# Kernel tuning notes

Hardware: AMD Instinct MI355X
Metric: run time of the kernel (lower is better)

Reference implementation:

```python
import jax, jax.numpy as jnp
import numpy as np

STEPS, BATCH = 2048, 512
INPUT_DIM = 16          # climate features after stripping flow channel
STORE_DIM = 8           # number of conceptual stores S
HIDDEN = 128
SLOW = 2                # SLOW_STORE index
RAIN_IDX = 0            # rain column within sliced climate inputs
OUT_DIM = STORE_DIM * (STORE_DIM + 2)   # flow_between_stores=True -> 80
IN_DIM_FLOWNET = INPUT_DIM + STORE_DIM  # 24


def setup_inputs() -> dict:
    key = jax.random.key(0)
    ks = jax.random.split(key, 10)
    hyd_input = jax.random.uniform(ks[0], (STEPS, BATCH, 1 + INPUT_DIM), dtype=jnp.float32)
    s = 0.05
    W0 = jax.random.normal(ks[1], (HIDDEN, IN_DIM_FLOWNET), dtype=jnp.float32) * s
    b0 = jax.random.normal(ks[2], (HIDDEN,), dtype=jnp.float32) * s
    W1 = jax.random.normal(ks[3], (HIDDEN, HIDDEN), dtype=jnp.float32) * s
    b1 = jax.random.normal(ks[4], (HIDDEN,), dtype=jnp.float32) * s
    W_in = jax.random.normal(ks[5], (STORE_DIM + 1, HIDDEN), dtype=jnp.float32) * s
    b_in = jax.random.normal(ks[6], (STORE_DIM + 1,), dtype=jnp.float32) * s
    W_out = jax.random.normal(ks[7], (OUT_DIM, HIDDEN), dtype=jnp.float32) * s
    b_out = jax.random.normal(ks[8], (OUT_DIM,), dtype=jnp.float32) * s - 3.0  # bias.data -= 3
    return {"hyd_input": hyd_input, "W0": W0, "b0": b0, "W1": W1, "b1": b1,
            "W_in": W_in, "b_in": b_in, "W_out": W_out, "b_out": b_out}


def reference(hyd_input, W0, b0, W1, b1, W_in, b_in, W_out, b_out):
    S = STORE_DIM
    flow = hyd_input[:, :, 0]          # [T, B] observed flow
    x = hyd_input[:, :, 1:]            # [T, B, F] climate forcings
    rain = x[:, :, RAIN_IDX]           # [T, B]
    # correct_init_baseflow: 25th percentile of observed flow over time, per batch elem
    baseflow = jnp.percentile(flow, 25.0, axis=0)  # [B]

    B = x.shape[1]
    stores0 = jnp.zeros((B, S), dtype=hyd_input.dtype).at[:, 1].set(1.0)  # init_stores

    def step(stores, inp):
        x_t, rain_t, is_first = inp
        # flownet: (num_layers=2) Linear -> ReLU (dropout is eval-mode identity)
        h = jnp.concatenate([x_t, 0.01 * stores], axis=1)      # [B, F+S]
        h = jax.nn.relu(h @ W0.T + b0)
        h = jax.nn.relu(h @ W1.T + b1)
        # inflow gating (softmax over S+1): distribute rain into stores
        a = jax.nn.softmax(h @ W_in.T + b_in, axis=-1)          # [B, S+1]
        stores = stores + a[:, 1:] * rain_t[:, None]
        # outflow fluxes (sigmoid), S*(S+2) = inter-store | escape | flow
        b = jax.nn.sigmoid(h @ W_out.T + b_out)                 # [B, S*(S+2)]
        # sequential inter-store transfers (order matters; S is small/fixed)
        for d in range(S):
            fb = b[:, d * S:(d + 1) * S] * stores               # [B, S]
            stores = (stores - fb).at[:, d].add(fb.sum(axis=1))
        escape = b[:, -2 * S:-S] * stores
        stores = stores - escape
        b_flow = b[:, -S:]
        flow_distn = b_flow * stores
        stores = stores - flow_distn
        # at i==0: overwrite slow store from baseflow / outflow coeff
        corrected = stores.at[:, SLOW].set(baseflow / jnp.maximum(b_flow[:, SLOW], 1e-5))
        stores = jnp.where(is_first, corrected, stores)
        return stores, flow_distn.sum(axis=1)

    is_first = jnp.arange(x.shape[0]) == 0
    _, flows = jax.lax.scan(step, stores0, (x, rain, is_first))
    return flows  # [T, B]
```

## Files before the change

kernel.cpp:

```cpp
#include <hip/hip_runtime.h>
#include <hip/hip_bf16.h>
#include <math.h>

#define STEPS 2048
#define BATCH 512

typedef __attribute__((ext_vector_type(8))) short short8;
typedef __attribute__((ext_vector_type(4))) short short4v;
typedef __attribute__((ext_vector_type(2))) short short2v;
typedef __attribute__((ext_vector_type(4))) float f32x4;

__device__ __forceinline__ short f2bf(float f) {
    union { float f; unsigned u; } v; v.f = f;
    unsigned u = v.u;
    return (short)((u + 0x7FFFu + ((u >> 16) & 1u)) >> 16);
}
__device__ __forceinline__ short2v pk2(float a, float b) {
    __hip_bfloat162 h = __float22bfloat162_rn(make_float2(a, b));
    union { __hip_bfloat162 h; short2v s; } u; u.h = h; return u.s;
}

__global__ __launch_bounds__(256) void baseflow_kernel(
    const float* __restrict__ hyd, float* __restrict__ bf)
{
    __shared__ float arr[STEPS];
    const int b = blockIdx.x;
    const int tid = threadIdx.x;
    for (int t = tid; t < STEPS; t += 256)
        arr[t] = hyd[(size_t)(t * BATCH + b) * 17];
    __syncthreads();
    for (int k = 2; k <= STEPS; k <<= 1) {
        for (int j = k >> 1; j > 0; j >>= 1) {
            for (int i = tid; i < STEPS; i += 256) {
                int ixj = i ^ j;
                if (ixj > i) {
                    float a = arr[i], c = arr[ixj];
                    bool up = ((i & k) == 0);
                    if (up ? (a > c) : (a < c)) { arr[i] = c; arr[ixj] = a; }
                }
            }
            __syncthreads();
        }
    }
    if (tid == 0) bf[b] = arr[511] + 0.75f * (arr[512] - arr[511]);
}

__global__ __launch_bounds__(256, 1) void hyd_step_kernel(
    const float* __restrict__ hyd,
    const float* __restrict__ W0,  const float* __restrict__ b0,
    const float* __restrict__ W1,  const float* __restrict__ b1,
    const float* __restrict__ Win, const float* __restrict__ bin,
    const float* __restrict__ Wout,const float* __restrict__ bout,
    const float* __restrict__ baseflow,
    float* __restrict__ out)
{
    __shared__ __align__(16) short h1F[256 * 8];
    __shared__ __align__(16) short h2F[256 * 8];
    __shared__ __align__(16) short ringX[16 * 4 * 8];
    __shared__ float ringR[16][2];
    __shared__ __align__(16) float hb[2][96];

    const int tid  = threadIdx.x;
    const int blk  = blockIdx.x;
    const int lane = tid & 63;
    const int wv   = tid >> 6;
    const int cn   = lane & 15;
    const int cg   = lane >> 4;
    const int col  = lane & 1;

    for (int i = tid; i < 256 * 8; i += 256) { h1F[i] = 0; h2F[i] = 0; }

    short8 a0[2]; f32x4 c0[2];
    short8 a1[2][4]; f32x4 c1[2];
    short8 ah[2][4]; f32x4 ch[2];
    #pragma unroll
    for (int i = 0; i < 2; ++i) {
        const int mt = 2 * wv + i;
        const int row = mt * 16 + cn;
        #pragma unroll
        for (int j = 0; j < 8; ++j) {
            int k = cg * 8 + j;
            a0[i][j] = (k < 24) ? f2bf(W0[row * 24 + k]) : (short)0;
        }
        #pragma unroll
        for (int kt = 0; kt < 4; ++kt)
            #pragma unroll
            for (int j = 0; j < 8; ++j)
                a1[i][kt][j] = f2bf(W1[row * 128 + kt * 32 + cg * 8 + j]);
        #pragma unroll
        for (int r = 0; r < 4; ++r) {
            int m = mt * 16 + cg * 4 + r;
            c0[i][r] = b0[m];
            c1[i][r] = b1[m];
        }
    }
    const int nht = (wv < 2) ? 2 : 1;
    int htile[2];
    htile[0] = (wv < 2) ? 2 * wv : 4 + (wv - 2);
    htile[1] = (wv < 2) ? 2 * wv + 1 : htile[0];
    #pragma unroll
    for (int i = 0; i < 2; ++i) {
        const int ht = htile[i];
        const int row = ht * 16 + cn;
        #pragma unroll
        for (int kt = 0; kt < 4; ++kt)
            #pragma unroll
            for (int j = 0; j < 8; ++j) {
                int k = kt * 32 + cg * 8 + j;
                float w = 0.f;
                if (row < 9)       w = Win[row * 128 + k];
                else if (row < 89) w = Wout[(row - 9) * 128 + k];
                ah[i][kt][j] = f2bf(w);
            }
        #pragma unroll
        for (int r = 0; r < 4; ++r) {
            int m = ht * 16 + cg * 4 + r;
            float bb = 0.f;
            if (m < 9)       bb = bin[m];
            else if (m < 89) bb = bout[m - 9];
            ch[i][r] = bb;
        }
    }

    float sreg[8];
    #pragma unroll
    for (int j = 0; j < 8; ++j) sreg[j] = (j == 1) ? 1.f : 0.f;
    const float bfv = baseflow[blk * 2 + col];
    short8 spack;
    #pragma unroll
    for (int jj = 0; jj < 4; ++jj) {
        short2v p = pk2(0.01f * sreg[2 * jj], 0.01f * sreg[2 * jj + 1]);
        spack[2 * jj] = p[0]; spack[2 * jj + 1] = p[1];
    }

    for (int tb = 0; tb < STEPS; tb += 16) {
        if (tid < 64) {
            const int tp = tid >> 2, c = (tid >> 1) & 1, g2 = tid & 1;
            const float* p = hyd + ((size_t)(tb + tp) * BATCH + blk * 2 + c) * 17 + 1 + g2 * 8;
            float v0 = p[0], v1 = p[1], v2 = p[2], v3 = p[3];
            float v4 = p[4], v5 = p[5], v6 = p[6], v7 = p[7];
            short8 w;
            short2v q0 = pk2(v0, v1), q1 = pk2(v2, v3), q2 = pk2(v4, v5), q3 = pk2(v6, v7);
            w[0] = q0[0]; w[1] = q0[1]; w[2] = q1[0]; w[3] = q1[1];
            w[4] = q2[0]; w[5] = q2[1]; w[6] = q3[0]; w[7] = q3[1];
            *(short8*)&ringX[(tp * 4 + g2 * 2 + c) * 8] = w;
        } else if (tid < 96) {
            const int l = tid - 64, tp = l >> 1, c = l & 1;
            ringR[tp][c] = hyd[((size_t)(tb + tp) * BATCH + blk * 2 + c) * 17 + 1];
        }
        __syncthreads();

        for (int tt = 0; tt < 16; ++tt) {
            const int t = tb + tt;

            const float rain = ringR[tt][col];

            short8 bfrag = 0;
            if (cn < 2) {
                if (cg < 2)        bfrag = *(const short8*)&ringX[(tt * 4 + cg * 2 + cn) * 8];
                else if (cg == 2)  bfrag = spack;
            }
            #pragma unroll
            for (int i = 0; i < 2; ++i) {
                f32x4 acc = __builtin_amdgcn_mfma_f32_16x16x32_bf16(a0[i], bfrag, c0[i], 0, 0, 0);
                if (cn < 2) {
                    int m0 = (2 * wv + i) * 16 + cg * 4;
                    short4v p;
                    short2v pa = pk2(fmaxf(acc[0], 0.f), fmaxf(acc[1], 0.f));
                    short2v pb = pk2(fmaxf(acc[2], 0.f), fmaxf(acc[3], 0.f));
                    p[0] = pa[0]; p[1] = pa[1]; p[2] = pb[0]; p[3] = pb[1];
                    *(short4v*)&h1F[((m0 >> 3) * 16 + cn) * 8 + (m0 & 7)] = p;
                }
            }
            __syncthreads();

            short8 bf1[4];
            #pragma unroll
            for (int kt = 0; kt < 4; ++kt)
                bf1[kt] = *(const short8*)&h1F[(kt * 64 + lane) * 8];
            #pragma unroll
            for (int i = 0; i < 2; ++i) {
                f32x4 acc = c1[i];
                #pragma unroll
                for (int kt = 0; kt < 4; ++kt)
                    acc = __builtin_amdgcn_mfma_f32_16x16x32_bf16(a1[i][kt], bf1[kt], acc, 0, 0, 0);
                if (cn < 2) {
                    int m0 = (2 * wv + i) * 16 + cg * 4;
                    short4v p;
                    short2v pa = pk2(fmaxf(acc[0], 0.f), fmaxf(acc[1], 0.f));
                    short2v pb = pk2(fmaxf(acc[2], 0.f), fmaxf(acc[3], 0.f));
                    p[0] = pa[0]; p[1] = pa[1]; p[2] = pb[0]; p[3] = pb[1];
                    *(short4v*)&h2F[((m0 >> 3) * 16 + cn) * 8 + (m0 & 7)] = p;
                }
            }
            __syncthreads();

            short8 bf2[4];
            #pragma unroll
            for (int kt = 0; kt < 4; ++kt)
                bf2[kt] = *(const short8*)&h2F[(kt * 64 + lane) * 8];
            #pragma unroll
            for (int i = 0; i < 2; ++i) {
                if (i < nht) {
                    f32x4 acc = ch[i];
                    #pragma unroll
                    for (int kt = 0; kt < 4; ++kt)
                        acc = __builtin_amdgcn_mfma_f32_16x16x32_bf16(ah[i][kt], bf2[kt], acc, 0, 0, 0);
                    if (cn < 2) {
                        const int ht = htile[i];
                        float4 o;
                        #pragma unroll
                        for (int r = 0; r < 4; ++r) {
                            int m = ht * 16 + cg * 4 + r;
                            float v = acc[r];
                            bool isl = (m < 9);
                            float em = __expf(isl ? v : -v);
                            float res = isl ? em : __builtin_amdgcn_rcpf(1.f + em);
                            ((float*)&o)[r] = res;
                        }
                        *(float4*)&hb[cn][ht * 16 + cg * 4] = o;
                    }
                }
            }
            __syncthreads();

            {
                float gv[92];
                const float4* hp = (const float4*)&hb[col][0];
                #pragma unroll
                for (int c2 = 0; c2 < 23; ++c2)
                    ((float4*)gv)[c2] = hp[c2];

                float den = ((gv[0] + gv[1]) + (gv[2] + gv[3])) +
                            ((gv[4] + gv[5]) + (gv[6] + gv[7])) + gv[8];
                float rr = rain * __builtin_amdgcn_rcpf(den);
                #pragma unroll
                for (int j = 0; j < 8; ++j) sreg[j] += gv[1 + j] * rr;

                #pragma unroll
                for (int d = 0; d < 8; ++d) {
                    float fb[8];
                    #pragma unroll
                    for (int j = 0; j < 8; ++j) fb[j] = gv[9 + d * 8 + j] * sreg[j];
                    float fs = ((fb[0] + fb[1]) + (fb[2] + fb[3])) +
                               ((fb[4] + fb[5]) + (fb[6] + fb[7]));
                    #pragma unroll
                    for (int j = 0; j < 8; ++j) sreg[j] -= fb[j];
                    sreg[d] += fs;
                }
                #pragma unroll
                for (int j = 0; j < 8; ++j) sreg[j] -= gv[73 + j] * sreg[j];
                float fd[8];
                #pragma unroll
                for (int j = 0; j < 8; ++j) fd[j] = gv[81 + j] * sreg[j];
                float fsum = ((fd[0] + fd[1]) + (fd[2] + fd[3])) +
                             ((fd[4] + fd[5]) + (fd[6] + fd[7]));
                #pragma unroll
                for (int j = 0; j < 8; ++j) sreg[j] -= fd[j];
                if (t == 0) sreg[2] = bfv / fmaxf(gv[83], 1e-5f);

                #pragma unroll
                for (int jj = 0; jj < 4; ++jj) {
                    short2v p = pk2(0.01f * sreg[2 * jj], 0.01f * sreg[2 * jj + 1]);
                    spack[2 * jj] = p[0]; spack[2 * jj + 1] = p[1];
                }
                if (tid < 2) out[(size_t)t * BATCH + blk * 2 + tid] = fsum;
            }
        }
    }
}

extern "C" void kernel_launch(void* const* d_in, const int* in_sizes, int n_in,
                              void* d_out, int out_size, void* d_ws, size_t ws_size,
                              hipStream_t stream)
{
    const float* hyd  = (const float*)d_in[0];
    const float* W0   = (const float*)d_in[1];
    const float* b0   = (const float*)d_in[2];
    const float* W1   = (const float*)d_in[3];
    const float* b1   = (const float*)d_in[4];
    const float* Win  = (const float*)d_in[5];
    const float* bin  = (const float*)d_in[6];
    const float* Wout = (const float*)d_in[7];
    const float* bout = (const float*)d_in[8];
    float* out = (float*)d_out;
    float* bf  = (float*)d_ws;

    baseflow_kernel<<<BATCH, 256, 0, stream>>>(hyd, bf);
    hyd_step_kernel<<<BATCH / 2, 256, 0, stream>>>(
        hyd, W0, b0, W1, b1, Win, bin, Wout, bout, bf, out);
}
```

Before: 3.380 ms.

## Process one batch element per block and spread store updates across lanes

Each block now handles a single batch column instead of two, doubling the grid and allowing two blocks per CU. The idea is to overlap the latency-bound recurrent chains of independent blocks on each CU. The sequential inter-store transfer loop moves from one thread doing all eight stores to eight lanes, one store each, with xor-shuffle reductions. The packed bf16 store vector is rebuilt from lane shuffles. The risks are lower MFMA column utilisation, more shuffle latency in the serial per-step path, and register pressure from the two-block launch bound.

Measured after the change: 4.384 ms. 29.7% more time.

```diff
diff --git a/kernel.cpp b/kernel.cpp
--- a/kernel.cpp
+++ b/kernel.cpp
@@ -14,6 +14,9 @@
     union { float f; unsigned u; } v; v.f = f;
     unsigned u = v.u;
     return (short)((u + 0x7FFFu + ((u >> 16) & 1u)) >> 16);
+}
+__device__ __forceinline__ unsigned f2bfu(float f) {
+    return (unsigned)(unsigned short)f2bf(f);
 }
 __device__ __forceinline__ short2v pk2(float a, float b) {
     __hip_bfloat162 h = __float22bfloat162_rn(make_float2(a, b));
@@ -45,7 +48,7 @@
     if (tid == 0) bf[b] = arr[511] + 0.75f * (arr[512] - arr[511]);
 }
 
-__global__ __launch_bounds__(256, 1) void hyd_step_kernel(
+__global__ __launch_bounds__(256, 2) void hyd_step_kernel(
     const float* __restrict__ hyd,
     const float* __restrict__ W0,  const float* __restrict__ b0,
     const float* __restrict__ W1,  const float* __restrict__ b1,
@@ -56,17 +59,17 @@
 {
     __shared__ __align__(16) short h1F[256 * 8];
     __shared__ __align__(16) short h2F[256 * 8];
-    __shared__ __align__(16) short ringX[16 * 4 * 8];
-    __shared__ float ringR[16][2];
-    __shared__ __align__(16) float hb[2][96];
+    __shared__ __align__(16) short ringX[16 * 2 * 8];
+    __shared__ float ringR[16];
+    __shared__ __align__(16) float hb[96];
 
     const int tid  = threadIdx.x;
-    const int blk  = blockIdx.x;
+    const int b    = blockIdx.x;
     const int lane = tid & 63;
     const int wv   = tid >> 6;
     const int cn   = lane & 15;
     const int cg   = lane >> 4;
-    const int col  = lane & 1;
+    const int j8   = lane & 7;
 
     for (int i = tid; i < 256 * 8; i += 256) { h1F[i] = 0; h2F[i] = 0; }
 
@@ -122,54 +125,49 @@
         }
     }
 
-    float sreg[8];
-    #pragma unroll
-    for (int j = 0; j < 8; ++j) sreg[j] = (j == 1) ? 1.f : 0.f;
-    const float bfv = baseflow[blk * 2 + col];
-    short8 spack;
-    #pragma unroll
-    for (int jj = 0; jj < 4; ++jj) {
-        short2v p = pk2(0.01f * sreg[2 * jj], 0.01f * sreg[2 * jj + 1]);
-        spack[2 * jj] = p[0]; spack[2 * jj + 1] = p[1];
-    }
+    float sj = (j8 == 1) ? 1.f : 0.f;
+    const float bfv = baseflow[b];
+    unsigned sp0 = (f2bfu(0.01f) << 16);
+    unsigned sp1 = 0, sp2 = 0, sp3 = 0;
 
     for (int tb = 0; tb < STEPS; tb += 16) {
-        if (tid < 64) {
-            const int tp = tid >> 2, c = (tid >> 1) & 1, g2 = tid & 1;
-            const float* p = hyd + ((size_t)(tb + tp) * BATCH + blk * 2 + c) * 17 + 1 + g2 * 8;
+        if (tid < 32) {
+            const int tp = tid >> 1, g2 = tid & 1;
+            const float* p = hyd + ((size_t)(tb + tp) * BATCH + b) * 17 + 1 + g2 * 8;
             float v0 = p[0], v1 = p[1], v2 = p[2], v3 = p[3];
             float v4 = p[4], v5 = p[5], v6 = p[6], v7 = p[7];
             short8 w;
             short2v q0 = pk2(v0, v1), q1 = pk2(v2, v3), q2 = pk2(v4, v5), q3 = pk2(v6, v7);
             w[0] = q0[0]; w[1] = q0[1]; w[2] = q1[0]; w[3] = q1[1];
             w[4] = q2[0]; w[5] = q2[1]; w[6] = q3[0]; w[7] = q3[1];
-            *(short8*)&ringX[(tp * 4 + g2 * 2 + c) * 8] = w;
-        } else if (tid < 96) {
-            const int l = tid - 64, tp = l >> 1, c = l & 1;
-            ringR[tp][c] = hyd[((size_t)(tb + tp) * BATCH + blk * 2 + c) * 17 + 1];
+            *(short8*)&ringX[(tp * 2 + g2) * 8] = w;
+        } else if (tid < 48) {
+            const int tp = tid - 32;
+            ringR[tp] = hyd[((size_t)(tb + tp) * BATCH + b) * 17 + 1];
         }
         __syncthreads();
 
         for (int tt = 0; tt < 16; ++tt) {
             const int t = tb + tt;
 
-            const float rain = ringR[tt][col];
-
-            short8 bfrag = 0;
-            if (cn < 2) {
-                if (cg < 2)        bfrag = *(const short8*)&ringX[(tt * 4 + cg * 2 + cn) * 8];
-                else if (cg == 2)  bfrag = spack;
+            short8 bfrag = (short8)0;
+            if (cg < 2) {
+                if (cn == 0) bfrag = *(const short8*)&ringX[(tt * 2 + cg) * 8];
+            } else if (cg == 2) {
+                union { unsigned u[4]; short8 s; } su;
+                su.u[0] = sp0; su.u[1] = sp1; su.u[2] = sp2; su.u[3] = sp3;
+                bfrag = su.s;
             }
             #pragma unroll
             for (int i = 0; i < 2; ++i) {
                 f32x4 acc = __builtin_amdgcn_mfma_f32_16x16x32_bf16(a0[i], bfrag, c0[i], 0, 0, 0);
-                if (cn < 2) {
+                if (cn == 0) {
                     int m0 = (2 * wv + i) * 16 + cg * 4;
                     short4v p;
                     short2v pa = pk2(fmaxf(acc[0], 0.f), fmaxf(acc[1], 0.f));
                     short2v pb = pk2(fmaxf(acc[2], 0.f), fmaxf(acc[3], 0.f));
                     p[0] = pa[0]; p[1] = pa[1]; p[2] = pb[0]; p[3] = pb[1];
-                    *(short4v*)&h1F[((m0 >> 3) * 16 + cn) * 8 + (m0 & 7)] = p;
+                    *(short4v*)&h1F[((m0 >> 3) * 16 + 0) * 8 + (m0 & 7)] = p;
                 }
             }
             __syncthreads();
@@ -184,16 +182,18 @@
                 #pragma unroll
                 for (int kt = 0; kt < 4; ++kt)
                     acc = __builtin_amdgcn_mfma_f32_16x16x32_bf16(a1[i][kt], bf1[kt], acc, 0, 0, 0);
-                if (cn < 2) {
+                if (cn == 0) {
                     int m0 = (2 * wv + i) * 16 + cg * 4;
                     short4v p;
                     short2v pa = pk2(fmaxf(acc[0], 0.f), fmaxf(acc[1], 0.f));
                     short2v pb = pk2(fmaxf(acc[2], 0.f), fmaxf(acc[3], 0.f));
                     p[0] = pa[0]; p[1] = pa[1]; p[2] = pb[0]; p[3] = pb[1];
-                    *(short4v*)&h2F[((m0 >> 3) * 16 + cn) * 8 + (m0 & 7)] = p;
-                }
-            }
-            __syncthreads();
+                    *(short4v*)&h2F[((m0 >> 3) * 16 + 0) * 8 + (m0 & 7)] = p;
+                }
+            }
+            __syncthreads();
+
+            const float rain = ringR[tt];
 
             short8 bf2[4];
             #pragma unroll
@@ -206,7 +206,7 @@
                     #pragma unroll
                     for (int kt = 0; kt < 4; ++kt)
                         acc = __builtin_amdgcn_mfma_f32_16x16x32_bf16(ah[i][kt], bf2[kt], acc, 0, 0, 0);
-                    if (cn < 2) {
+                    if (cn == 0) {
                         const int ht = htile[i];
                         float4 o;
                         #pragma unroll
@@ -215,56 +215,61 @@
                             float v = acc[r];
                             bool isl = (m < 9);
                             float em = __expf(isl ? v : -v);
-                            float res = isl ? em : __builtin_amdgcn_rcpf(1.f + em);
-                            ((float*)&o)[r] = res;
+                            ((float*)&o)[r] = isl ? em : __builtin_amdgcn_rcpf(1.f + em);
                         }
-                        *(float4*)&hb[cn][ht * 16 + cg * 4] = o;
+                        *(float4*)&hb[ht * 16 + cg * 4] = o;
                     }
                 }
             }
             __syncthreads();
 
             {
-                float gv[92];
-                const float4* hp = (const float4*)&hb[col][0];
+                float ej  = hb[1 + j8];
+                float e0  = hb[0];
+                float Bd[8];
                 #pragma unroll
-                for (int c2 = 0; c2 < 23; ++c2)
-                    ((float4*)gv)[c2] = hp[c2];
-
-                float den = ((gv[0] + gv[1]) + (gv[2] + gv[3])) +
-                            ((gv[4] + gv[5]) + (gv[6] + gv[7])) + gv[8];
+                for (int d = 0; d < 8; ++d) Bd[d] = hb[9 + 8 * d + j8];
+                float esc = hb[73 + j8];
+                float bfl = hb[81 + j8];
+
+                float den = ej;
+                den += __shfl_xor(den, 1, 8);
+                den += __shfl_xor(den, 2, 8);
+                den += __shfl_xor(den, 4, 8);
+                den += e0;
                 float rr = rain * __builtin_amdgcn_rcpf(den);
-                #pragma unroll
-                for (int j = 0; j < 8; ++j) sreg[j] += gv[1 + j] * rr;
+                sj += ej * rr;
 
                 #pragma unroll
                 for (int d = 0; d < 8; ++d) {
-                    float fb[8];
-                    #pragma unroll
-                    for (int j = 0; j < 8; ++j) fb[j] = gv[9 + d * 8 + j] * sreg[j];
-                    float fs = ((fb[0] + fb[1]) + (fb[2] + fb[3])) +
-                               ((fb[4] + fb[5]) + (fb[6] + fb[7]));
-                    #pragma unroll
-                    for (int j = 0; j < 8; ++j) sreg[j] -= fb[j];
-                    sreg[d] += fs;
-                }
-                #pragma unroll
-                for (int j = 0; j < 8; ++j) sreg[j] -= gv[73 + j] * sreg[j];
-                float fd[8];
-                #pragma unroll
-                for (int j = 0; j < 8; ++j) fd[j] = gv[81 + j] * sreg[j];
-                float fsum = ((fd[0] + fd[1]) + (fd[2] + fd[3])) +
-                             ((fd[4] + fd[5]) + (fd[6] + fd[7]));
-                #pragma unroll
-                for (int j = 0; j < 8; ++j) sreg[j] -= fd[j];
-                if (t == 0) sreg[2] = bfv / fmaxf(gv[83], 1e-5f);
-
-                #pragma unroll
-                for (int jj = 0; jj < 4; ++jj) {
-                    short2v p = pk2(0.01f * sreg[2 * jj], 0.01f * sreg[2 * jj + 1]);
-                    spack[2 * jj] = p[0]; spack[2 * jj + 1] = p[1];
-                }
-                if (tid < 2) out[(size_t)t * BATCH + blk * 2 + tid] = fsum;
+                    float fb = Bd[d] * sj;
+                    float fs = fb;
+                    fs += __shfl_xor(fs, 1, 8);
+                    fs += __shfl_xor(fs, 2, 8);
+                    fs += __shfl_xor(fs, 4, 8);
+                    sj -= fb;
+                    if (j8 == d) sj += fs;
+                }
+                sj -= esc * sj;
+                float fd = bfl * sj;
+                float fsum = fd;
+                fsum += __shfl_xor(fsum, 1, 8);
+                fsum += __shfl_xor(fsum, 2, 8);
+                fsum += __shfl_xor(fsum, 4, 8);
+                sj -= fd;
+                if (t == 0) {
+                    float bflS = __shfl(bfl, 2, 8);
+                    if (j8 == 2) sj = bfv / fmaxf(bflS, 1e-5f);
+                }
+                if (tid == 0) out[(size_t)t * BATCH + b] = fsum;
+
+                unsigned myb = f2bfu(0.01f * sj);
+                unsigned prt = (unsigned)__shfl_xor((int)myb, 1, 8);
+                unsigned pair = (myb & 0xFFFFu) | (prt << 16);
+                sp0 = pair;
+                sp1 = (unsigned)__shfl_xor((int)pair, 2, 8);
+                sp2 = (unsigned)__shfl_xor((int)pair, 4, 8);
+                sp3 = (unsigned)__shfl_xor((int)sp1, 4, 8);
             }
         }
     }
@@ -287,6 +292,6 @@
     float* bf  = (float*)d_ws;
 
     baseflow_kernel<<<BATCH, 256, 0, stream>>>(hyd, bf);
-    hyd_step_kernel<<<BATCH / 2, 256, 0, stream>>>(
+    hyd_step_kernel<<<BATCH, 256, 0, stream>>>(
         hyd, W0, b0, W1, b1, Win, bin, Wout, bout, bf, out);
 }
```

## Use one wavefront per 16 batch columns to drop block barriers in recurrence

Applied to the files above, without the earlier changes.

Restructures the recurrent step kernel from 256-thread blocks handling 2 batch columns across four waves into single-wave blocks handling 16 columns. All weight tiles now live in one wave's registers, so the per-step __syncthreads barriers disappear and all 16 MFMA columns carry useful work instead of only 2. The b0 bias and the 0.01 store scale are folded into the W0 fragment through a constant-one input column. Next-step inputs are prefetched directly from global memory, replacing the shared-memory ring. The cost is much higher register pressure, since every wave holds all weights, and only 32 waves run on the GPU, so each step's serial MFMA chain becomes longer.

Measured after the change: 5.466 ms. +61.7%, slower.

```diff
diff --git a/kernel.cpp b/kernel.cpp
--- a/kernel.cpp
+++ b/kernel.cpp
@@ -4,6 +4,8 @@
 
 #define STEPS 2048
 #define BATCH 512
+#define SH 136
+#define SB 100
 
 typedef __attribute__((ext_vector_type(8))) short short8;
 typedef __attribute__((ext_vector_type(4))) short short4v;
@@ -45,7 +47,7 @@
     if (tid == 0) bf[b] = arr[511] + 0.75f * (arr[512] - arr[511]);
 }
 
-__global__ __launch_bounds__(256, 1) void hyd_step_kernel(
+__global__ __launch_bounds__(64, 1) void hyd_step_kernel(
     const float* __restrict__ hyd,
     const float* __restrict__ W0,  const float* __restrict__ b0,
     const float* __restrict__ W1,  const float* __restrict__ b1,
@@ -54,219 +56,198 @@
     const float* __restrict__ baseflow,
     float* __restrict__ out)
 {
-    __shared__ __align__(16) short h1F[256 * 8];
-    __shared__ __align__(16) short h2F[256 * 8];
-    __shared__ __align__(16) short ringX[16 * 4 * 8];
-    __shared__ float ringR[16][2];
-    __shared__ __align__(16) float hb[2][96];
-
-    const int tid  = threadIdx.x;
-    const int blk  = blockIdx.x;
-    const int lane = tid & 63;
-    const int wv   = tid >> 6;
-    const int cn   = lane & 15;
-    const int cg   = lane >> 4;
-    const int col  = lane & 1;
-
-    for (int i = tid; i < 256 * 8; i += 256) { h1F[i] = 0; h2F[i] = 0; }
-
-    short8 a0[2]; f32x4 c0[2];
-    short8 a1[2][4]; f32x4 c1[2];
-    short8 ah[2][4]; f32x4 ch[2];
-    #pragma unroll
-    for (int i = 0; i < 2; ++i) {
-        const int mt = 2 * wv + i;
-        const int row = mt * 16 + cn;
+    __shared__ __align__(16) short h1F[16 * SH];
+    __shared__ __align__(16) short h2F[16 * SH];
+    __shared__ __align__(16) float hb[16 * SB];
+
+    const int lane = threadIdx.x;
+    const int n = lane & 15;
+    const int q = lane >> 4;
+    const int bcol = blockIdx.x * 16 + n;
+
+    short8 a0[8];
+    short8 a1[8][4]; f32x4 c1[8];
+    short8 ah[6][4]; f32x4 ch[6];
+    #pragma unroll
+    for (int mt = 0; mt < 8; ++mt) {
+        const int row = mt * 16 + n;
         #pragma unroll
         for (int j = 0; j < 8; ++j) {
-            int k = cg * 8 + j;
-            a0[i][j] = (k < 24) ? f2bf(W0[row * 24 + k]) : (short)0;
+            const int k = q * 8 + j;
+            float w;
+            if (k < 16)       w = W0[row * 24 + k];
+            else if (k < 24)  w = 0.01f * W0[row * 24 + k];
+            else if (k == 24) w = b0[row];
+            else              w = 0.f;
+            a0[mt][j] = f2bf(w);
         }
         #pragma unroll
         for (int kt = 0; kt < 4; ++kt)
             #pragma unroll
             for (int j = 0; j < 8; ++j)
-                a1[i][kt][j] = f2bf(W1[row * 128 + kt * 32 + cg * 8 + j]);
-        #pragma unroll
-        for (int r = 0; r < 4; ++r) {
-            int m = mt * 16 + cg * 4 + r;
-            c0[i][r] = b0[m];
-            c1[i][r] = b1[m];
-        }
-    }
-    const int nht = (wv < 2) ? 2 : 1;
-    int htile[2];
-    htile[0] = (wv < 2) ? 2 * wv : 4 + (wv - 2);
-    htile[1] = (wv < 2) ? 2 * wv + 1 : htile[0];
-    #pragma unroll
-    for (int i = 0; i < 2; ++i) {
-        const int ht = htile[i];
-        const int row = ht * 16 + cn;
+                a1[mt][kt][j] = f2bf(W1[row * 128 + kt * 32 + q * 8 + j]);
+        #pragma unroll
+        for (int r = 0; r < 4; ++r) c1[mt][r] = b1[mt * 16 + q * 4 + r];
+    }
+    #pragma unroll
+    for (int ht = 0; ht < 6; ++ht) {
+        const int row = ht * 16 + n;
         #pragma unroll
         for (int kt = 0; kt < 4; ++kt)
             #pragma unroll
             for (int j = 0; j < 8; ++j) {
-                int k = kt * 32 + cg * 8 + j;
+                const int k = kt * 32 + q * 8 + j;
                 float w = 0.f;
                 if (row < 9)       w = Win[row * 128 + k];
                 else if (row < 89) w = Wout[(row - 9) * 128 + k];
-                ah[i][kt][j] = f2bf(w);
+                ah[ht][kt][j] = f2bf(w);
             }
         #pragma unroll
         for (int r = 0; r < 4; ++r) {
-            int m = ht * 16 + cg * 4 + r;
+            const int m = ht * 16 + q * 4 + r;
             float bb = 0.f;
             if (m < 9)       bb = bin[m];
             else if (m < 89) bb = bout[m - 9];
-            ch[i][r] = bb;
+            ch[ht][r] = bb;
         }
     }
 
     float sreg[8];
     #pragma unroll
     for (int j = 0; j < 8; ++j) sreg[j] = (j == 1) ? 1.f : 0.f;
-    const float bfv = baseflow[blk * 2 + col];
-    short8 spack;
+    short8 sp;
     #pragma unroll
     for (int jj = 0; jj < 4; ++jj) {
-        short2v p = pk2(0.01f * sreg[2 * jj], 0.01f * sreg[2 * jj + 1]);
-        spack[2 * jj] = p[0]; spack[2 * jj + 1] = p[1];
-    }
-
-    for (int tb = 0; tb < STEPS; tb += 16) {
-        if (tid < 64) {
-            const int tp = tid >> 2, c = (tid >> 1) & 1, g2 = tid & 1;
-            const float* p = hyd + ((size_t)(tb + tp) * BATCH + blk * 2 + c) * 17 + 1 + g2 * 8;
-            float v0 = p[0], v1 = p[1], v2 = p[2], v3 = p[3];
-            float v4 = p[4], v5 = p[5], v6 = p[6], v7 = p[7];
-            short8 w;
-            short2v q0 = pk2(v0, v1), q1 = pk2(v2, v3), q2 = pk2(v4, v5), q3 = pk2(v6, v7);
-            w[0] = q0[0]; w[1] = q0[1]; w[2] = q1[0]; w[3] = q1[1];
-            w[4] = q2[0]; w[5] = q2[1]; w[6] = q3[0]; w[7] = q3[1];
-            *(short8*)&ringX[(tp * 4 + g2 * 2 + c) * 8] = w;
-        } else if (tid < 96) {
-            const int l = tid - 64, tp = l >> 1, c = l & 1;
-            ringR[tp][c] = hyd[((size_t)(tb + tp) * BATCH + blk * 2 + c) * 17 + 1];
-        }
-        __syncthreads();
-
-        for (int tt = 0; tt < 16; ++tt) {
-            const int t = tb + tt;
-
-            const float rain = ringR[tt][col];
-
-            short8 bfrag = 0;
-            if (cn < 2) {
-                if (cg < 2)        bfrag = *(const short8*)&ringX[(tt * 4 + cg * 2 + cn) * 8];
-                else if (cg == 2)  bfrag = spack;
-            }
-            #pragma unroll
-            for (int i = 0; i < 2; ++i) {
-                f32x4 acc = __builtin_amdgcn_mfma_f32_16x16x32_bf16(a0[i], bfrag, c0[i], 0, 0, 0);
-                if (cn < 2) {
-                    int m0 = (2 * wv + i) * 16 + cg * 4;
-                    short4v p;
-                    short2v pa = pk2(fmaxf(acc[0], 0.f), fmaxf(acc[1], 0.f));
-                    short2v pb = pk2(fmaxf(acc[2], 0.f), fmaxf(acc[3], 0.f));
-                    p[0] = pa[0]; p[1] = pa[1]; p[2] = pb[0]; p[3] = pb[1];
-                    *(short4v*)&h1F[((m0 >> 3) * 16 + cn) * 8 + (m0 & 7)] = p;
-                }
-            }
-            __syncthreads();
-
-            short8 bf1[4];
+        short2v p = pk2(sreg[2 * jj], sreg[2 * jj + 1]);
+        sp[2 * jj] = p[0]; sp[2 * jj + 1] = p[1];
+    }
+    short8 onef = (short8)0; onef[0] = (short)0x3F80;
+    const float bfv = baseflow[bcol];
+
+    const float* colbase = hyd + (size_t)bcol * 17 + 1;
+    float xf[8] = {0, 0, 0, 0, 0, 0, 0, 0};
+    if (q < 2) {
+        #pragma unroll
+        for (int j = 0; j < 8; ++j) xf[j] = colbase[q * 8 + j];
+    }
+    float rainN = colbase[0];
+
+    #pragma unroll 1
+    for (int t = 0; t < STEPS; ++t) {
+        const float rain = rainN;
+        short8 xq;
+        #pragma unroll
+        for (int jj = 0; jj < 4; ++jj) {
+            short2v p = pk2(xf[2 * jj], xf[2 * jj + 1]);
+            xq[2 * jj] = p[0]; xq[2 * jj + 1] = p[1];
+        }
+        const int tn = (t + 1 < STEPS) ? (t + 1) : t;
+        const float* pnext = colbase + (size_t)tn * (BATCH * 17);
+        float nx[8] = {0, 0, 0, 0, 0, 0, 0, 0};
+        if (q < 2) {
+            #pragma unroll
+            for (int j = 0; j < 8; ++j) nx[j] = pnext[q * 8 + j];
+        }
+        const float nrain = pnext[0];
+
+        short8 bf0 = (q < 2) ? xq : ((q == 2) ? sp : onef);
+        #pragma unroll
+        for (int mt = 0; mt < 8; ++mt) {
+            f32x4 z = {0.f, 0.f, 0.f, 0.f};
+            f32x4 acc = __builtin_amdgcn_mfma_f32_16x16x32_bf16(a0[mt], bf0, z, 0, 0, 0);
+            short4v p;
+            short2v pa = pk2(fmaxf(acc[0], 0.f), fmaxf(acc[1], 0.f));
+            short2v pb = pk2(fmaxf(acc[2], 0.f), fmaxf(acc[3], 0.f));
+            p[0] = pa[0]; p[1] = pa[1]; p[2] = pb[0]; p[3] = pb[1];
+            *(short4v*)&h1F[n * SH + mt * 16 + q * 4] = p;
+        }
+
+        short8 bh1[4];
+        #pragma unroll
+        for (int kt = 0; kt < 4; ++kt)
+            bh1[kt] = *(const short8*)&h1F[n * SH + kt * 32 + q * 8];
+        #pragma unroll
+        for (int mt = 0; mt < 8; ++mt) {
+            f32x4 acc = c1[mt];
             #pragma unroll
             for (int kt = 0; kt < 4; ++kt)
-                bf1[kt] = *(const short8*)&h1F[(kt * 64 + lane) * 8];
-            #pragma unroll
-            for (int i = 0; i < 2; ++i) {
-                f32x4 acc = c1[i];
+                acc = __builtin_amdgcn_mfma_f32_16x16x32_bf16(a1[mt][kt], bh1[kt], acc, 0, 0, 0);
+            short4v p;
+            short2v pa = pk2(fmaxf(acc[0], 0.f), fmaxf(acc[1], 0.f));
+            short2v pb = pk2(fmaxf(acc[2], 0.f), fmaxf(acc[3], 0.f));
+            p[0] = pa[0]; p[1] = pa[1]; p[2] = pb[0]; p[3] = pb[1];
+            *(short4v*)&h2F[n * SH + mt * 16 + q * 4] = p;
+        }
+
+        short8 bh2[4];
+        #pragma unroll
+        for (int kt = 0; kt < 4; ++kt)
+            bh2[kt] = *(const short8*)&h2F[n * SH + kt * 32 + q * 8];
+        #pragma unroll
+        for (int ht = 0; ht < 6; ++ht) {
+            f32x4 acc = ch[ht];
+            #pragma unroll
+            for (int kt = 0; kt < 4; ++kt)
+                acc = __builtin_amdgcn_mfma_f32_16x16x32_bf16(ah[ht][kt], bh2[kt], acc, 0, 0, 0);
+            float4 o;
+            #pragma unroll
+            for (int r = 0; r < 4; ++r) {
+                const int m = ht * 16 + q * 4 + r;
+                const float v = acc[r];
+                const bool isl = (m < 9);
+                const float em = __expf(isl ? v : -v);
+                ((float*)&o)[r] = isl ? em : __builtin_amdgcn_rcpf(1.f + em);
+            }
+            *(float4*)&hb[n * SB + ht * 16 + q * 4] = o;
+        }
+
+        {
+            float gv[92];
+            const float4* hp = (const float4*)&hb[n * SB];
+            #pragma unroll
+            for (int c2 = 0; c2 < 23; ++c2)
+                ((float4*)gv)[c2] = hp[c2];
+
+            float den = ((gv[0] + gv[1]) + (gv[2] + gv[3])) +
+                        ((gv[4] + gv[5]) + (gv[6] + gv[7])) + gv[8];
+            float rr = rain * __builtin_amdgcn_rcpf(den);
+            #pragma unroll
+            for (int j = 0; j < 8; ++j) sreg[j] += gv[1 + j] * rr;
+
+            #pragma unroll
+            for (int d = 0; d < 8; ++d) {
+                float fb[8];
                 #pragma unroll
-                for (int kt = 0; kt < 4; ++kt)
-                    acc = __builtin_amdgcn_mfma_f32_16x16x32_bf16(a1[i][kt], bf1[kt], acc, 0, 0, 0);
-                if (cn < 2) {
-                    int m0 = (2 * wv + i) * 16 + cg * 4;
-                    short4v p;
-                    short2v pa = pk2(fmaxf(acc[0], 0.f), fmaxf(acc[1], 0.f));
-                    short2v pb = pk2(fmaxf(acc[2], 0.f), fmaxf(acc[3], 0.f));
-                    p[0] = pa[0]; p[1] = pa[1]; p[2] = pb[0]; p[3] = pb[1];
-                    *(short4v*)&h2F[((m0 >> 3) * 16 + cn) * 8 + (m0 & 7)] = p;
-                }
-            }
-            __syncthreads();
-
-            short8 bf2[4];
-            #pragma unroll
-            for (int kt = 0; kt < 4; ++kt)
-                bf2[kt] = *(const short8*)&h2F[(kt * 64 + lane) * 8];
-            #pragma unroll
-            for (int i = 0; i < 2; ++i) {
-                if (i < nht) {
-                    f32x4 acc = ch[i];
-                    #pragma unroll
-                    for (int kt = 0; kt < 4; ++kt)
-                        acc = __builtin_amdgcn_mfma_f32_16x16x32_bf16(ah[i][kt], bf2[kt], acc, 0, 0, 0);
-                    if (cn < 2) {
-                        const int ht = htile[i];
-                        float4 o;
-                        #pragma unroll
-                        for (int r = 0; r < 4; ++r) {
-                            int m = ht * 16 + cg * 4 + r;
-                            float v = acc[r];
-                            bool isl = (m < 9);
-                            float em = __expf(isl ? v : -v);
-                            float res = isl ? em : __builtin_amdgcn_rcpf(1.f + em);
-                            ((float*)&o)[r] = res;
-                        }
-                        *(float4*)&hb[cn][ht * 16 + cg * 4] = o;
-                    }
-                }
-            }
-            __syncthreads();
-
-            {
-                float gv[92];
-                const float4* hp = (const float4*)&hb[col][0];
+                for (int j = 0; j < 8; ++j) fb[j] = gv[9 + d * 8 + j] * sreg[j];
+                float fs = ((fb[0] + fb[1]) + (fb[2] + fb[3])) +
+                           ((fb[4] + fb[5]) + (fb[6] + fb[7]));
                 #pragma unroll
-                for (int c2 = 0; c2 < 23; ++c2)
-                    ((float4*)gv)[c2] = hp[c2];
-
-                float den = ((gv[0] + gv[1]) + (gv[2] + gv[3])) +
-                            ((gv[4] + gv[5]) + (gv[6] + gv[7])) + gv[8];
-                float rr = rain * __builtin_amdgcn_rcpf(den);
-                #pragma unroll
-                for (int j = 0; j < 8; ++j) sreg[j] += gv[1 + j] * rr;
-
-                #pragma unroll
-                for (int d = 0; d < 8; ++d) {
-                    float fb[8];
-                    #pragma unroll
-                    for (int j = 0; j < 8; ++j) fb[j] = gv[9 + d * 8 + j] * sreg[j];
-                    float fs = ((fb[0] + fb[1]) + (fb[2] + fb[3])) +
-                               ((fb[4] + fb[5]) + (fb[6] + fb[7]));
-                    #pragma unroll
-                    for (int j = 0; j < 8; ++j) sreg[j] -= fb[j];
-                    sreg[d] += fs;
-                }
-                #pragma unroll
-                for (int j = 0; j < 8; ++j) sreg[j] -= gv[73 + j] * sreg[j];
-                float fd[8];
-                #pragma unroll
-                for (int j = 0; j < 8; ++j) fd[j] = gv[81 + j] * sreg[j];
-                float fsum = ((fd[0] + fd[1]) + (fd[2] + fd[3])) +
-                             ((fd[4] + fd[5]) + (fd[6] + fd[7]));
-                #pragma unroll
-                for (int j = 0; j < 8; ++j) sreg[j] -= fd[j];
-                if (t == 0) sreg[2] = bfv / fmaxf(gv[83], 1e-5f);
-
-                #pragma unroll
-                for (int jj = 0; jj < 4; ++jj) {
-                    short2v p = pk2(0.01f * sreg[2 * jj], 0.01f * sreg[2 * jj + 1]);
-                    spack[2 * jj] = p[0]; spack[2 * jj + 1] = p[1];
-                }
-                if (tid < 2) out[(size_t)t * BATCH + blk * 2 + tid] = fsum;
-            }
-        }
+                for (int j = 0; j < 8; ++j) sreg[j] -= fb[j];
+                sreg[d] += fs;
+            }
+            #pragma unroll
+            for (int j = 0; j < 8; ++j) sreg[j] -= gv[73 + j] * sreg[j];
+            float fd[8];
+            #pragma unroll
+            for (int j = 0; j < 8; ++j) fd[j] = gv[81 + j] * sreg[j];
+            float fsum = ((fd[0] + fd[1]) + (fd[2] + fd[3])) +
+                         ((fd[4] + fd[5]) + (fd[6] + fd[7]));
+            #pragma unroll
+            for (int j = 0; j < 8; ++j) sreg[j] -= fd[j];
+            if (t == 0) sreg[2] = bfv / fmaxf(gv[83], 1e-5f);
+
+            if (q == 0) out[(size_t)t * BATCH + bcol] = fsum;
+
+            #pragma unroll
+            for (int jj = 0; jj < 4; ++jj) {
+                short2v p = pk2(sreg[2 * jj], sreg[2 * jj + 1]);
+                sp[2 * jj] = p[0]; sp[2 * jj + 1] = p[1];
+            }
+        }
+
+        #pragma unroll
+        for (int j = 0; j < 8; ++j) xf[j] = nx[j];
+        rainN = nrain;
     }
 }
 
@@ -287,6 +268,6 @@
     float* bf  = (float*)d_ws;
 
     baseflow_kernel<<<BATCH, 256, 0, stream>>>(hyd, bf);
-    hyd_step_kernel<<<BATCH / 2, 256, 0, stream>>>(
+    hyd_step_kernel<<<BATCH / 16, 64, 0, stream>>>(
         hyd, W0, b0, W1, b1, Win, bin, Wout, bout, bf, out);
 }
```

## Prefetch next input chunk into registers, split MFMA chains, batch output stores

Applied to the files above, without the earlier changes.

Loads for the next 16-step block of climate and rain inputs are issued into registers right after the current block is staged in shared memory, so global-load latency overlaps the 16 sequential steps. Each 4-deep MFMA accumulation chain is split into two independent 2-deep chains that are summed at the end, to shorten the dependent latency on the serial critical path. Per-step output writes are buffered in shared memory and flushed once per block. The costs are extra registers and a slightly different floating-point summation order.

New measurement: 3.481 ms. 1.03x slower.

```diff
diff --git a/kernel.cpp b/kernel.cpp
--- a/kernel.cpp
+++ b/kernel.cpp
@@ -59,6 +59,7 @@
     __shared__ __align__(16) short ringX[16 * 4 * 8];
     __shared__ float ringR[16][2];
     __shared__ __align__(16) float hb[2][96];
+    __shared__ float outS[16][2];
 
     const int tid  = threadIdx.x;
     const int blk  = blockIdx.x;
@@ -133,29 +134,50 @@
         spack[2 * jj] = p[0]; spack[2 * jj + 1] = p[1];
     }
 
+    const int rtp = tid >> 2, rc = (tid >> 1) & 1, rg2 = tid & 1;
+    const int rl  = tid - 64, rtpR = rl >> 1, rcR = rl & 1;
+    float xr[8];
+    #pragma unroll
+    for (int j = 0; j < 8; ++j) xr[j] = 0.f;
+    float rr = 0.f;
+    if (tid < 64) {
+        const float* p = hyd + ((size_t)rtp * BATCH + blk * 2 + rc) * 17 + 1 + rg2 * 8;
+        #pragma unroll
+        for (int j = 0; j < 8; ++j) xr[j] = p[j];
+    } else if (tid < 96) {
+        rr = hyd[((size_t)rtpR * BATCH + blk * 2 + rcR) * 17 + 1];
+    }
+
     for (int tb = 0; tb < STEPS; tb += 16) {
         if (tid < 64) {
-            const int tp = tid >> 2, c = (tid >> 1) & 1, g2 = tid & 1;
-            const float* p = hyd + ((size_t)(tb + tp) * BATCH + blk * 2 + c) * 17 + 1 + g2 * 8;
-            float v0 = p[0], v1 = p[1], v2 = p[2], v3 = p[3];
-            float v4 = p[4], v5 = p[5], v6 = p[6], v7 = p[7];
             short8 w;
-            short2v q0 = pk2(v0, v1), q1 = pk2(v2, v3), q2 = pk2(v4, v5), q3 = pk2(v6, v7);
+            short2v q0 = pk2(xr[0], xr[1]), q1 = pk2(xr[2], xr[3]);
+            short2v q2 = pk2(xr[4], xr[5]), q3 = pk2(xr[6], xr[7]);
             w[0] = q0[0]; w[1] = q0[1]; w[2] = q1[0]; w[3] = q1[1];
             w[4] = q2[0]; w[5] = q2[1]; w[6] = q3[0]; w[7] = q3[1];
-            *(short8*)&ringX[(tp * 4 + g2 * 2 + c) * 8] = w;
+            *(short8*)&ringX[(rtp * 4 + rg2 * 2 + rc) * 8] = w;
         } else if (tid < 96) {
-            const int l = tid - 64, tp = l >> 1, c = l & 1;
-            ringR[tp][c] = hyd[((size_t)(tb + tp) * BATCH + blk * 2 + c) * 17 + 1];
+            ringR[rtpR][rcR] = rr;
         }
         __syncthreads();
+
+        {
+            const int ntb = (tb + 16 < STEPS) ? (tb + 16) : tb;
+            if (tid < 64) {
+                const float* p = hyd + ((size_t)(ntb + rtp) * BATCH + blk * 2 + rc) * 17 + 1 + rg2 * 8;
+                #pragma unroll
+                for (int j = 0; j < 8; ++j) xr[j] = p[j];
+            } else if (tid < 96) {
+                rr = hyd[((size_t)(ntb + rtpR) * BATCH + blk * 2 + rcR) * 17 + 1];
+            }
+        }
 
         for (int tt = 0; tt < 16; ++tt) {
             const int t = tb + tt;
 
             const float rain = ringR[tt][col];
 
-            short8 bfrag = 0;
+            short8 bfrag = (short8)0;
             if (cn < 2) {
                 if (cg < 2)        bfrag = *(const short8*)&ringX[(tt * 4 + cg * 2 + cn) * 8];
                 else if (cg == 2)  bfrag = spack;
@@ -180,10 +202,12 @@
                 bf1[kt] = *(const short8*)&h1F[(kt * 64 + lane) * 8];
             #pragma unroll
             for (int i = 0; i < 2; ++i) {
-                f32x4 acc = c1[i];
-                #pragma unroll
-                for (int kt = 0; kt < 4; ++kt)
-                    acc = __builtin_amdgcn_mfma_f32_16x16x32_bf16(a1[i][kt], bf1[kt], acc, 0, 0, 0);
+                f32x4 z = {0.f, 0.f, 0.f, 0.f};
+                f32x4 aA = __builtin_amdgcn_mfma_f32_16x16x32_bf16(a1[i][0], bf1[0], c1[i], 0, 0, 0);
+                aA = __builtin_amdgcn_mfma_f32_16x16x32_bf16(a1[i][1], bf1[1], aA, 0, 0, 0);
+                f32x4 aB = __builtin_amdgcn_mfma_f32_16x16x32_bf16(a1[i][2], bf1[2], z, 0, 0, 0);
+                aB = __builtin_amdgcn_mfma_f32_16x16x32_bf16(a1[i][3], bf1[3], aB, 0, 0, 0);
+                f32x4 acc = aA + aB;
                 if (cn < 2) {
                     int m0 = (2 * wv + i) * 16 + cg * 4;
                     short4v p;
@@ -202,10 +226,12 @@
             #pragma unroll
             for (int i = 0; i < 2; ++i) {
                 if (i < nht) {
-                    f32x4 acc = ch[i];
-                    #pragma unroll
-                    for (int kt = 0; kt < 4; ++kt)
-                        acc = __builtin_amdgcn_mfma_f32_16x16x32_bf16(ah[i][kt], bf2[kt], acc, 0, 0, 0);
+                    f32x4 z = {0.f, 0.f, 0.f, 0.f};
+                    f32x4 aA = __builtin_amdgcn_mfma_f32_16x16x32_bf16(ah[i][0], bf2[0], ch[i], 0, 0, 0);
+                    aA = __builtin_amdgcn_mfma_f32_16x16x32_bf16(ah[i][1], bf2[1], aA, 0, 0, 0);
+                    f32x4 aB = __builtin_amdgcn_mfma_f32_16x16x32_bf16(ah[i][2], bf2[2], z, 0, 0, 0);
+                    aB = __builtin_amdgcn_mfma_f32_16x16x32_bf16(ah[i][3], bf2[3], aB, 0, 0, 0);
+                    f32x4 acc = aA + aB;
                     if (cn < 2) {
                         const int ht = htile[i];
                         float4 o;
@@ -215,8 +241,7 @@
                             float v = acc[r];
                             bool isl = (m < 9);
                             float em = __expf(isl ? v : -v);
-                            float res = isl ? em : __builtin_amdgcn_rcpf(1.f + em);
-                            ((float*)&o)[r] = res;
+                            ((float*)&o)[r] = isl ? em : __builtin_amdgcn_rcpf(1.f + em);
                         }
                         *(float4*)&hb[cn][ht * 16 + cg * 4] = o;
                     }
@@ -233,9 +258,9 @@
 
                 float den = ((gv[0] + gv[1]) + (gv[2] + gv[3])) +
                             ((gv[4] + gv[5]) + (gv[6] + gv[7])) + gv[8];
-                float rr = rain * __builtin_amdgcn_rcpf(den);
-                #pragma unroll
-                for (int j = 0; j < 8; ++j) sreg[j] += gv[1 + j] * rr;
+                float rr2 = rain * __builtin_amdgcn_rcpf(den);
+                #pragma unroll
+                for (int j = 0; j < 8; ++j) sreg[j] += gv[1 + j] * rr2;
 
                 #pragma unroll
                 for (int d = 0; d < 8; ++d) {
@@ -259,13 +284,19 @@
                 for (int j = 0; j < 8; ++j) sreg[j] -= fd[j];
                 if (t == 0) sreg[2] = bfv / fmaxf(gv[83], 1e-5f);
 
+                if (tid < 2) outS[tt][tid] = fsum;
+
                 #pragma unroll
                 for (int jj = 0; jj < 4; ++jj) {
                     short2v p = pk2(0.01f * sreg[2 * jj], 0.01f * sreg[2 * jj + 1]);
                     spack[2 * jj] = p[0]; spack[2 * jj + 1] = p[1];
                 }
-                if (tid < 2) out[(size_t)t * BATCH + blk * 2 + tid] = fsum;
-            }
+            }
+        }
+
+        if (tid < 32) {
+            const int tp = tid >> 1, c = tid & 1;
+            out[(size_t)(tb + tp) * BATCH + blk * 2 + c] = outS[tp][c];
         }
     }
 }
```
